# Optimization experiments

Hardware: AMD Instinct MI355X
Metric: run time of the kernel (lower is better)

## Reference

```python
import jax, jax.numpy as jnp
import numpy as np

TIME_PENALTY = 0.01
PONDER_EPS = 0.01
TIME_LIMIT = 16
BATCH, INPUT_SIZE, HIDDEN_SIZE = 4096, 1024, 1024


def setup_inputs() -> dict:
    key = jax.random.key(0)
    ks = jax.random.split(key, 8)
    s_in = 1.0 / np.sqrt(INPUT_SIZE + 1)
    s_h = 1.0 / np.sqrt(HIDDEN_SIZE)
    return {
        "inputs": jax.random.normal(ks[0], (BATCH, INPUT_SIZE), jnp.float32),
        "hidden": jax.random.normal(ks[1], (BATCH, HIDDEN_SIZE), jnp.float32),
        # RNNCell params (input size = INPUT_SIZE + 1 for the first-step flag)
        "W_ih": jax.random.uniform(ks[2], (HIDDEN_SIZE, INPUT_SIZE + 1), jnp.float32, -s_in, s_in),
        "b_ih": jax.random.uniform(ks[3], (HIDDEN_SIZE,), jnp.float32, -s_in, s_in),
        "W_hh": jax.random.uniform(ks[4], (HIDDEN_SIZE, HIDDEN_SIZE), jnp.float32, -s_h, s_h),
        "b_hh": jax.random.uniform(ks[5], (HIDDEN_SIZE,), jnp.float32, -s_h, s_h),
        # halting unit: Linear(hidden_size, 1), bias initialized to -1.0
        "W_halt": jax.random.uniform(ks[6], (1, HIDDEN_SIZE), jnp.float32, -s_h, s_h),
        "b_halt": jnp.full((1,), -1.0, jnp.float32),
    }


def _act_forward(inputs, hidden, W_ih, b_ih, W_hh, b_hh, W_halt, b_halt):
    B = inputs.shape[0]
    H = W_hh.shape[0]
    dt = inputs.dtype
    budget = jnp.asarray(1.0 - PONDER_EPS, dt)
    # input projection: the last input column is the first-step flag, so
    # step_inputs @ W_ih^T == inputs @ W_ih[:, :-1]^T + flag * W_ih[:, -1]
    x_base = inputs @ W_ih[:, :-1].T + b_ih  # (B, H)
    flag_col = W_ih[:, -1]                    # (H,)
    flags = (jnp.arange(TIME_LIMIT - 1) == 0).astype(dt)

    def step(carry, flag):
        h, halt_accum, cont, tot_h, tot_rem, tot_steps = carry
        h = jnp.tanh(x_base + flag * flag_col + h @ W_hh.T + b_hh)  # (B, H)
        step_halt = jax.nn.sigmoid(h @ W_halt.T + b_halt)           # (B, 1)
        masked_halt = jnp.where(cont, step_halt, 0.0)
        # halt accumulator is detached in the original (torch.no_grad)
        halt_accum = halt_accum + jax.lax.stop_gradient(masked_halt)
        ending = cont & (halt_accum + step_halt > budget)
        cont = cont & (~ending)
        tot_steps = tot_steps + cont.astype(dt)
        masked_rem = jnp.where(ending, 1.0 - halt_accum, 0.0)
        combined = masked_halt + masked_rem
        tot_h = tot_h + combined * h
        tot_rem = tot_rem + masked_halt
        return (h, halt_accum, cont, tot_h, tot_rem, tot_steps), None

    init = (
        hidden,
        jnp.zeros((B, 1), dt),
        jnp.ones((B, 1), bool),
        jnp.zeros((B, H), dt),
        jnp.zeros((B, 1), dt),
        jnp.zeros((B, 1), dt),
    )
    (h, halt_accum, cont, tot_h, tot_rem, tot_steps), _ = jax.lax.scan(step, init, flags)
    # for-else branch: elements still continuing after the loop get the remainder
    # (zero-contribution if everything halted early, matching the early break)
    tot_h = tot_h + jnp.where(cont, 1.0 - halt_accum, 0.0) * h
    ponder_cost = -TIME_PENALTY * tot_rem.mean()
    return tot_h, ponder_cost, tot_steps + 1.0


def reference(inputs, hidden, W_ih, b_ih, W_hh, b_hh, W_halt, b_halt):
    return _act_forward(inputs, hidden, W_ih, b_ih, W_hh, b_hh, W_halt, b_halt)
```

## Files before the change

kernel.cpp:

```cpp
#include <hip/hip_runtime.h>
#include <math.h>

#define BATCH 4096
#define HID   1024
#define KDIM  1024
#define NSTEP 15
#define KV    3072
#define NCHUNK (KV / 64)

#define TMM 128
#define TNN 64
#define LDAH 72

typedef _Float16 half8 __attribute__((ext_vector_type(8)));
typedef float floatx4 __attribute__((ext_vector_type(4)));

__device__ __forceinline__ _Float16 f16hi(float x) { return (_Float16)x; }

__global__ __launch_bounds__(256) void setup_kernel(
    const float* __restrict__ W_ih, const float* __restrict__ W_hh,
    const float* __restrict__ inputs, const float* __restrict__ hidden,
    _Float16* __restrict__ B3ih, _Float16* __restrict__ B3hh,
    _Float16* __restrict__ Ihi, _Float16* __restrict__ Ilo,
    _Float16* __restrict__ Hhi, _Float16* __restrict__ Hlo,
    float* __restrict__ flagcol, int* __restrict__ list0, int* __restrict__ counts,
    float* __restrict__ halt_accum, float* __restrict__ tot_rem) {
    size_t idx = (size_t)blockIdx.x * 256 + threadIdx.x;
    {
        float x = inputs[idx];
        _Float16 h = f16hi(x);
        Ihi[idx] = h; Ilo[idx] = (_Float16)(x - (float)h);
        float y = hidden[idx];
        _Float16 g = f16hi(y);
        Hhi[idx] = g; Hlo[idx] = (_Float16)(y - (float)g);
    }
    if (idx < (size_t)KDIM * KDIM) {
        int n = (int)(idx >> 10), k = (int)(idx & 1023);
        float w = W_hh[idx];
        _Float16 hi = f16hi(w);
        _Float16 lo = (_Float16)(w - (float)hi);
        size_t base = (size_t)n * KV;
        B3hh[base + k] = hi; B3hh[base + 1024 + k] = lo; B3hh[base + 2048 + k] = hi;
        float w2 = W_ih[(size_t)n * 1025 + k];
        _Float16 hi2 = f16hi(w2);
        _Float16 lo2 = (_Float16)(w2 - (float)hi2);
        B3ih[base + k] = hi2; B3ih[base + 1024 + k] = lo2; B3ih[base + 2048 + k] = hi2;
    }
    if (idx < BATCH) { list0[idx] = idx; halt_accum[idx] = 0.f; tot_rem[idx] = 0.f; }
    if (idx < KDIM) flagcol[idx] = W_ih[idx * 1025 + 1024];
    if (idx < 16) counts[idx] = (idx == 0) ? BATCH : 0;
}

__global__ __launch_bounds__(256) void mfma_step_kernel(
    const _Float16* __restrict__ Ahi, const _Float16* __restrict__ Alo,
    const _Float16* __restrict__ B3, const float* __restrict__ bias,
    const float* __restrict__ xbase, const float* __restrict__ flagcol, float flag,
    const int* __restrict__ list, const int* __restrict__ pcount,
    float* __restrict__ hout, _Float16* __restrict__ houthi, _Float16* __restrict__ houtlo,
    float* __restrict__ xout, int mode) {
    int count = pcount ? *pcount : BATCH;
    int row0 = blockIdx.x * TMM;
    if (row0 >= count) return;
    int col0 = blockIdx.y * TNN;

    __shared__ _Float16 Asm[2][TMM][LDAH];
    __shared__ _Float16 Bsm[2][TNN][LDAH];

    int t = threadIdx.x;
    int lane = t & 63, w = t >> 6;
    int wm = (w & 1) * 64, wn = (w >> 1) * 32;

    int arw[4], aq8[4]; size_t aoff[4];
#pragma unroll
    for (int l = 0; l < 4; l++) {
        int q = t + l * 256;
        int r = q >> 3, qk = q & 7;
        arw[l] = r; aq8[l] = qk * 8;
        int rr = row0 + r;
        int g = (rr < count) ? (list ? list[rr] : rr) : 0;
        aoff[l] = (size_t)g * KDIM + qk * 8;
    }
    int brw[2], bq8[2]; size_t boff[2];
#pragma unroll
    for (int l = 0; l < 2; l++) {
        int q = t + l * 256;
        int r = q >> 3, qk = q & 7;
        brw[l] = r; bq8[l] = qk * 8;
        boff[l] = (size_t)(col0 + r) * KV + qk * 8;
    }

    floatx4 acc[4][2];
#pragma unroll
    for (int i = 0; i < 4; i++)
#pragma unroll
        for (int j = 0; j < 2; j++) acc[i][j] = (floatx4)(0.f);

    int l15 = lane & 15, l4 = lane >> 4;

    half8 av[4], bv[2];
#pragma unroll
    for (int l = 0; l < 4; l++) av[l] = *(const half8*)(Ahi + aoff[l]);
#pragma unroll
    for (int l = 0; l < 2; l++) bv[l] = *(const half8*)(B3 + boff[l]);
#pragma unroll
    for (int l = 0; l < 4; l++) *(half8*)(&Asm[0][arw[l]][aq8[l]]) = av[l];
#pragma unroll
    for (int l = 0; l < 2; l++) *(half8*)(&Bsm[0][brw[l]][bq8[l]]) = bv[l];
    __syncthreads();

    int p = 0;
    for (int it = 0; it < NCHUNK; it++) {
        if (it + 1 < NCHUNK) {
            int k0v = (it + 1) << 6;
            const _Float16* Asrc = (k0v < 2048) ? Ahi : Alo;
            int kp = k0v & 1023;
#pragma unroll
            for (int l = 0; l < 4; l++) av[l] = *(const half8*)(Asrc + aoff[l] + kp);
#pragma unroll
            for (int l = 0; l < 2; l++) bv[l] = *(const half8*)(B3 + boff[l] + k0v);
        }
#pragma unroll
        for (int ks = 0; ks < 2; ks++) {
            int ko = ks * 32 + l4 * 8;
            half8 af[4], bf[2];
#pragma unroll
            for (int fi = 0; fi < 4; fi++)
                af[fi] = *(const half8*)(&Asm[p][wm + fi * 16 + l15][ko]);
#pragma unroll
            for (int fj = 0; fj < 2; fj++)
                bf[fj] = *(const half8*)(&Bsm[p][wn + fj * 16 + l15][ko]);
#pragma unroll
            for (int fi = 0; fi < 4; fi++)
#pragma unroll
                for (int fj = 0; fj < 2; fj++)
                    acc[fi][fj] = __builtin_amdgcn_mfma_f32_16x16x32_f16(
                        af[fi], bf[fj], acc[fi][fj], 0, 0, 0);
        }
        if (it + 1 < NCHUNK) {
            int q = p ^ 1;
#pragma unroll
            for (int l = 0; l < 4; l++) *(half8*)(&Asm[q][arw[l]][aq8[l]]) = av[l];
#pragma unroll
            for (int l = 0; l < 2; l++) *(half8*)(&Bsm[q][brw[l]][bq8[l]]) = bv[l];
        }
        __syncthreads();
        p ^= 1;
    }

#pragma unroll
    for (int fi = 0; fi < 4; fi++) {
#pragma unroll
        for (int rr = 0; rr < 4; rr++) {
            int lm = wm + fi * 16 + l4 * 4 + rr;
            int grd = row0 + lm;
            if (grd >= count) continue;
            int g = list ? list[grd] : grd;
#pragma unroll
            for (int fj = 0; fj < 2; fj++) {
                int c = col0 + wn + fj * 16 + l15;
                float v = acc[fi][fj][rr];
                if (mode == 0) {
                    xout[(size_t)g * KDIM + c] = v + bias[c];
                } else {
                    v += xbase[(size_t)g * KDIM + c] + flag * flagcol[c] + bias[c];
                    v = tanhf(v);
                    hout[(size_t)g * KDIM + c] = v;
                    _Float16 hi = f16hi(v);
                    houthi[(size_t)g * KDIM + c] = hi;
                    houtlo[(size_t)g * KDIM + c] = (_Float16)(v - (float)hi);
                }
            }
        }
    }
}

__global__ __launch_bounds__(256) void halt_kernel(
    const float* __restrict__ h, const float* __restrict__ W_halt,
    const float* __restrict__ b_halt,
    const int* __restrict__ list, const int* __restrict__ pcount,
    int* __restrict__ list_next, int* __restrict__ pcount_next,
    float* __restrict__ halt_accum, float* __restrict__ tot_rem,
    float* __restrict__ tot_h, float* __restrict__ steps_out,
    int stepnum, int first) {
    int count = *pcount;
    int wid = threadIdx.x >> 6, lane = threadIdx.x & 63;
    int r = blockIdx.x * 4 + wid;
    if (r >= count) return;
    int row = list[r];
    const float* hr = h + (size_t)row * HID;

    float dot = 0.f;
#pragma unroll
    for (int q = 0; q < 4; q++) {
        int c = q * 256 + lane * 4;
        float4 hv = *(const float4*)(hr + c);
        float4 wv = *(const float4*)(W_halt + c);
        dot += hv.x * wv.x + hv.y * wv.y + hv.z * wv.z + hv.w * wv.w;
    }
#pragma unroll
    for (int off = 32; off > 0; off >>= 1) dot += __shfl_down(dot, off);

    float combined = 0.f;
    if (lane == 0) {
        float p = 1.f / (1.f + expf(-(dot + b_halt[0])));
        float S = halt_accum[row] + p;
        halt_accum[row] = S;
        tot_rem[row] += p;
        bool ending = (S + p) > 0.99f;
        if (ending) {
            combined = p + (1.f - S);
            steps_out[row] = (float)stepnum;
        } else {
            combined = p;
            int idx = atomicAdd(pcount_next, 1);
            list_next[idx] = row;
        }
    }
    combined = __shfl(combined, 0);

    float* th = tot_h + (size_t)row * HID;
#pragma unroll
    for (int q = 0; q < 4; q++) {
        int c = q * 256 + lane * 4;
        float4 hv = *(const float4*)(hr + c);
        float4 ov;
        if (first) {
            ov.x = combined * hv.x; ov.y = combined * hv.y;
            ov.z = combined * hv.z; ov.w = combined * hv.w;
        } else {
            ov = *(const float4*)(th + c);
            ov.x += combined * hv.x; ov.y += combined * hv.y;
            ov.z += combined * hv.z; ov.w += combined * hv.w;
        }
        *(float4*)(th + c) = ov;
    }
}

__global__ __launch_bounds__(256) void epilogue_kernel(
    const float* __restrict__ h, const int* __restrict__ list,
    const int* __restrict__ pcount, const float* __restrict__ halt_accum,
    const float* __restrict__ tot_rem,
    float* __restrict__ tot_h, float* __restrict__ steps_out,
    float* __restrict__ ponder) {
    if (blockIdx.x == 1024) {
        __shared__ float red[4];
        int t = threadIdx.x;
        float v = 0.f;
#pragma unroll
        for (int i = 0; i < 16; i++) v += tot_rem[t + i * 256];
#pragma unroll
        for (int off = 32; off > 0; off >>= 1) v += __shfl_down(v, off);
        int lane = t & 63, wid = t >> 6;
        if (lane == 0) red[wid] = v;
        __syncthreads();
        if (t == 0) ponder[0] = (red[0] + red[1] + red[2] + red[3]) * (-0.01f / 4096.f);
        return;
    }
    int count = *pcount;
    int wid = threadIdx.x >> 6, lane = threadIdx.x & 63;
    int r = blockIdx.x * 4 + wid;
    if (r >= count) return;
    int row = list[r];
    float cmb = 1.f - halt_accum[row];
    if (lane == 0) steps_out[row] = 16.f;
    const float* hr = h + (size_t)row * HID;
    float* th = tot_h + (size_t)row * HID;
#pragma unroll
    for (int q = 0; q < 4; q++) {
        int c = q * 256 + lane * 4;
        float4 hv = *(const float4*)(hr + c);
        float4 ov = *(const float4*)(th + c);
        ov.x += cmb * hv.x; ov.y += cmb * hv.y;
        ov.z += cmb * hv.z; ov.w += cmb * hv.w;
        *(float4*)(th + c) = ov;
    }
}

extern "C" void kernel_launch(void* const* d_in, const int* in_sizes, int n_in,
                              void* d_out, int out_size, void* d_ws, size_t ws_size,
                              hipStream_t stream) {
    const float* inputs = (const float*)d_in[0];
    const float* hidden = (const float*)d_in[1];
    const float* W_ih   = (const float*)d_in[2];
    const float* b_ih   = (const float*)d_in[3];
    const float* W_hh   = (const float*)d_in[4];
    const float* b_hh   = (const float*)d_in[5];
    const float* W_halt = (const float*)d_in[6];
    const float* b_halt = (const float*)d_in[7];
    float* out = (float*)d_out;

    float* ws = (float*)d_ws;
    const size_t NM = (size_t)BATCH * HID;
    float* xbase = ws;
    float* h     = xbase + NM;
    _Float16* B3ih = (_Float16*)(h + NM);
    _Float16* B3hh = B3ih + (size_t)HID * KV;
    _Float16* Ahi0 = B3hh + (size_t)HID * KV;
    _Float16* Alo0 = Ahi0 + NM;
    _Float16* Ahi1 = Alo0 + NM;
    _Float16* Alo1 = Ahi1 + NM;
    float* flagcol = (float*)(Alo1 + NM);
    float* halt_accum = flagcol + KDIM;
    float* tot_rem = halt_accum + BATCH;
    int* list0 = (int*)(tot_rem + BATCH);
    int* list1 = list0 + BATCH;
    int* counts = list1 + BATCH;

    _Float16* Ahi[2] = {Ahi0, Ahi1};
    _Float16* Alo[2] = {Alo0, Alo1};
    int* lists[2] = {list0, list1};

    float* tot_h = out;
    float* ponder = out + NM;
    float* steps_out = ponder + 1;

    setup_kernel<<<16384, 256, 0, stream>>>(W_ih, W_hh, inputs, hidden,
                                            B3ih, B3hh, Ahi1, Alo1, Ahi0, Alo0,
                                            flagcol, list0, counts, halt_accum, tot_rem);

    mfma_step_kernel<<<dim3(32, 16), 256, 0, stream>>>(
        Ahi1, Alo1, B3ih, b_ih, nullptr, nullptr, 0.f, nullptr, nullptr,
        nullptr, nullptr, nullptr, xbase, 0);

    for (int t = 0; t < NSTEP; t++) {
        mfma_step_kernel<<<dim3(32, 16), 256, 0, stream>>>(
            Ahi[t & 1], Alo[t & 1], B3hh, b_hh, xbase, flagcol,
            (t == 0) ? 1.f : 0.f, lists[t & 1], counts + t,
            h, Ahi[(t + 1) & 1], Alo[(t + 1) & 1], nullptr, 1);
        halt_kernel<<<1024, 256, 0, stream>>>(h, W_halt, b_halt,
                                              lists[t & 1], counts + t,
                                              lists[(t + 1) & 1], counts + t + 1,
                                              halt_accum, tot_rem, tot_h, steps_out,
                                              t + 1, (t == 0) ? 1 : 0);
    }
    epilogue_kernel<<<1025, 256, 0, stream>>>(h, lists[1], counts + 15,
                                              halt_accum, tot_rem, tot_h, steps_out, ponder);
}
```

Before: 736.3 us.

## Deepen GEMM prefetch to two register stages with LDS-only barriers

Reworks the GEMM main loop to keep two chunks of global loads in flight, using even and odd register sets, so global latency is hidden across two MFMA chunks instead of one. It also replaces __syncthreads with a custom barrier that waits only on LDS counters (lgkmcnt) and not on outstanding global loads. This lets prefetched global loads stay pending across barriers. The cost is more register pressure from the extra staging buffers, which could lower occupancy.

```diff
diff --git a/kernel.cpp b/kernel.cpp
--- a/kernel.cpp
+++ b/kernel.cpp
@@ -16,6 +16,12 @@
 typedef float floatx4 __attribute__((ext_vector_type(4)));
 
 __device__ __forceinline__ _Float16 f16hi(float x) { return (_Float16)x; }
+
+__device__ __forceinline__ void barrier_ls() {
+    asm volatile("s_waitcnt lgkmcnt(0)" ::: "memory");
+    __builtin_amdgcn_s_barrier();
+    asm volatile("" ::: "memory");
+}
 
 __global__ __launch_bounds__(256) void setup_kernel(
     const float* __restrict__ W_ih, const float* __restrict__ W_hh,
@@ -97,55 +103,65 @@
 
     int l15 = lane & 15, l4 = lane >> 4;
 
-    half8 av[4], bv[2];
-#pragma unroll
-    for (int l = 0; l < 4; l++) av[l] = *(const half8*)(Ahi + aoff[l]);
-#pragma unroll
-    for (int l = 0; l < 2; l++) bv[l] = *(const half8*)(B3 + boff[l]);
-#pragma unroll
-    for (int l = 0; l < 4; l++) *(half8*)(&Asm[0][arw[l]][aq8[l]]) = av[l];
-#pragma unroll
-    for (int l = 0; l < 2; l++) *(half8*)(&Bsm[0][brw[l]][bq8[l]]) = bv[l];
-    __syncthreads();
-
-    int p = 0;
-    for (int it = 0; it < NCHUNK; it++) {
-        if (it + 1 < NCHUNK) {
-            int k0v = (it + 1) << 6;
-            const _Float16* Asrc = (k0v < 2048) ? Ahi : Alo;
-            int kp = k0v & 1023;
-#pragma unroll
-            for (int l = 0; l < 4; l++) av[l] = *(const half8*)(Asrc + aoff[l] + kp);
-#pragma unroll
-            for (int l = 0; l < 2; l++) bv[l] = *(const half8*)(B3 + boff[l] + k0v);
-        }
-#pragma unroll
-        for (int ks = 0; ks < 2; ks++) {
-            int ko = ks * 32 + l4 * 8;
-            half8 af[4], bf[2];
-#pragma unroll
-            for (int fi = 0; fi < 4; fi++)
-                af[fi] = *(const half8*)(&Asm[p][wm + fi * 16 + l15][ko]);
-#pragma unroll
-            for (int fj = 0; fj < 2; fj++)
-                bf[fj] = *(const half8*)(&Bsm[p][wn + fj * 16 + l15][ko]);
-#pragma unroll
-            for (int fi = 0; fi < 4; fi++)
-#pragma unroll
-                for (int fj = 0; fj < 2; fj++)
-                    acc[fi][fj] = __builtin_amdgcn_mfma_f32_16x16x32_f16(
-                        af[fi], bf[fj], acc[fi][fj], 0, 0, 0);
-        }
-        if (it + 1 < NCHUNK) {
-            int q = p ^ 1;
-#pragma unroll
-            for (int l = 0; l < 4; l++) *(half8*)(&Asm[q][arw[l]][aq8[l]]) = av[l];
-#pragma unroll
-            for (int l = 0; l < 2; l++) *(half8*)(&Bsm[q][brw[l]][bq8[l]]) = bv[l];
-        }
-        __syncthreads();
-        p ^= 1;
-    }
+    half8 avE[4], bvE[2];
+    half8 avO[4], bvO[2];
+
+#define ISSUE(avS, bvS, c) do {                                               \
+        int k0v_ = (c) << 6;                                                  \
+        const _Float16* Asrc_ = (k0v_ < 2048) ? Ahi : Alo;  \
+        int kp_ = k0v_ & 1023;                                                \
+        _Pragma("unroll")                                                     \
+        for (int l = 0; l < 4; l++) avS[l] = *(const half8*)(Asrc_ + aoff[l] + kp_); \
+        _Pragma("unroll")                                                     \
+        for (int l = 0; l < 2; l++) bvS[l] = *(const half8*)(B3 + boff[l] + k0v_);   \
+    } while (0)
+
+#define LDSW(buf, avS, bvS) do {                                              \
+        _Pragma("unroll")                                                     \
+        for (int l = 0; l < 4; l++) *(half8*)(&Asm[buf][arw[l]][aq8[l]]) = avS[l]; \
+        _Pragma("unroll")                                                     \
+        for (int l = 0; l < 2; l++) *(half8*)(&Bsm[buf][brw[l]][bq8[l]]) = bvS[l]; \
+    } while (0)
+
+#define MFMA_CHUNK(buf) do {                                                  \
+        _Pragma("unroll")                                                     \
+        for (int ks = 0; ks < 2; ks++) {                                      \
+            int ko = ks * 32 + l4 * 8;                                        \
+            half8 af[4], bf[2];                                               \
+            _Pragma("unroll")                                                 \
+            for (int fi = 0; fi < 4; fi++)                                    \
+                af[fi] = *(const half8*)(&Asm[buf][wm + fi * 16 + l15][ko]);  \
+            _Pragma("unroll")                                                 \
+            for (int fj = 0; fj < 2; fj++)                                    \
+                bf[fj] = *(const half8*)(&Bsm[buf][wn + fj * 16 + l15][ko]);  \
+            _Pragma("unroll")                                                 \
+            for (int fi = 0; fi < 4; fi++)                                    \
+                _Pragma("unroll")                                             \
+                for (int fj = 0; fj < 2; fj++)                                \
+                    acc[fi][fj] = __builtin_amdgcn_mfma_f32_16x16x32_f16(     \
+                        af[fi], bf[fj], acc[fi][fj], 0, 0, 0);                \
+        }                                                                     \
+    } while (0)
+
+    ISSUE(avE, bvE, 0);
+    ISSUE(avO, bvO, 1);
+    LDSW(0, avE, bvE);
+    barrier_ls();
+
+    for (int it = 0; it < NCHUNK; it += 2) {
+        if (it + 2 < NCHUNK) ISSUE(avE, bvE, it + 2);
+        MFMA_CHUNK(0);
+        LDSW(1, avO, bvO);
+        barrier_ls();
+        if (it + 3 < NCHUNK) ISSUE(avO, bvO, it + 3);
+        MFMA_CHUNK(1);
+        if (it + 2 < NCHUNK) LDSW(0, avE, bvE);
+        barrier_ls();
+    }
+
+#undef ISSUE
+#undef LDSW
+#undef MFMA_CHUNK
 
 #pragma unroll
     for (int fi = 0; fi < 4; fi++) {
```

New measurement: 738.5 us. About the same (+0.3%).

## Add per-wave tiled GEMM path for small active-row counts in step kernel

Applied to the files above, without the earlier changes.

The recurrent step kernel now switches on the active-row count. Above a threshold it keeps the shared-memory 128x64 block tile. Below it, each wavefront independently computes a 64x64 tile, reading operands straight from global memory with a three-stage register prefetch and no LDS or barriers. This spreads the shrinking tail batches across more independent waves to improve utilisation once many rows have halted. The cost is more register pressure in the fused kernel and redundant global loads that are not shared through LDS.

```diff
diff --git a/kernel.cpp b/kernel.cpp
--- a/kernel.cpp
+++ b/kernel.cpp
@@ -7,6 +7,7 @@
 #define NSTEP 15
 #define KV    3072
 #define NCHUNK (KV / 64)
+#define TAILTHRESH 1536
 
 #define TMM 128
 #define TNN 64
@@ -59,115 +60,207 @@
     float* __restrict__ hout, _Float16* __restrict__ houthi, _Float16* __restrict__ houtlo,
     float* __restrict__ xout, int mode) {
     int count = pcount ? *pcount : BATCH;
-    int row0 = blockIdx.x * TMM;
-    if (row0 >= count) return;
-    int col0 = blockIdx.y * TNN;
+    int t = threadIdx.x;
+    int lane = t & 63, w = t >> 6;
+    int l15 = lane & 15, l4 = lane >> 4;
 
     __shared__ _Float16 Asm[2][TMM][LDAH];
     __shared__ _Float16 Bsm[2][TNN][LDAH];
 
-    int t = threadIdx.x;
-    int lane = t & 63, w = t >> 6;
-    int wm = (w & 1) * 64, wn = (w >> 1) * 32;
-
-    int arw[4], aq8[4]; size_t aoff[4];
-#pragma unroll
-    for (int l = 0; l < 4; l++) {
-        int q = t + l * 256;
-        int r = q >> 3, qk = q & 7;
-        arw[l] = r; aq8[l] = qk * 8;
-        int rr = row0 + r;
-        int g = (rr < count) ? (list ? list[rr] : rr) : 0;
-        aoff[l] = (size_t)g * KDIM + qk * 8;
-    }
-    int brw[2], bq8[2]; size_t boff[2];
-#pragma unroll
-    for (int l = 0; l < 2; l++) {
-        int q = t + l * 256;
-        int r = q >> 3, qk = q & 7;
-        brw[l] = r; bq8[l] = qk * 8;
-        boff[l] = (size_t)(col0 + r) * KV + qk * 8;
-    }
-
-    floatx4 acc[4][2];
-#pragma unroll
-    for (int i = 0; i < 4; i++)
-#pragma unroll
-        for (int j = 0; j < 2; j++) acc[i][j] = (floatx4)(0.f);
-
-    int l15 = lane & 15, l4 = lane >> 4;
-
-    half8 av[4], bv[2];
-#pragma unroll
-    for (int l = 0; l < 4; l++) av[l] = *(const half8*)(Ahi + aoff[l]);
-#pragma unroll
-    for (int l = 0; l < 2; l++) bv[l] = *(const half8*)(B3 + boff[l]);
-#pragma unroll
-    for (int l = 0; l < 4; l++) *(half8*)(&Asm[0][arw[l]][aq8[l]]) = av[l];
-#pragma unroll
-    for (int l = 0; l < 2; l++) *(half8*)(&Bsm[0][brw[l]][bq8[l]]) = bv[l];
-    __syncthreads();
-
-    int p = 0;
-    for (int it = 0; it < NCHUNK; it++) {
-        if (it + 1 < NCHUNK) {
-            int k0v = (it + 1) << 6;
-            const _Float16* Asrc = (k0v < 2048) ? Ahi : Alo;
-            int kp = k0v & 1023;
-#pragma unroll
-            for (int l = 0; l < 4; l++) av[l] = *(const half8*)(Asrc + aoff[l] + kp);
-#pragma unroll
-            for (int l = 0; l < 2; l++) bv[l] = *(const half8*)(B3 + boff[l] + k0v);
-        }
-#pragma unroll
-        for (int ks = 0; ks < 2; ks++) {
-            int ko = ks * 32 + l4 * 8;
-            half8 af[4], bf[2];
-#pragma unroll
-            for (int fi = 0; fi < 4; fi++)
-                af[fi] = *(const half8*)(&Asm[p][wm + fi * 16 + l15][ko]);
-#pragma unroll
-            for (int fj = 0; fj < 2; fj++)
-                bf[fj] = *(const half8*)(&Bsm[p][wn + fj * 16 + l15][ko]);
-#pragma unroll
-            for (int fi = 0; fi < 4; fi++)
+    if (count >= TAILTHRESH) {
+        int bx = blockIdx.x & 31, by = blockIdx.x >> 5;
+        int row0 = bx * TMM;
+        if (row0 >= count) return;
+        int col0 = by * TNN;
+        int wm = (w & 1) * 64, wn = (w >> 1) * 32;
+
+        int arw[4], aq8[4]; size_t aoff[4];
+#pragma unroll
+        for (int l = 0; l < 4; l++) {
+            int q = t + l * 256;
+            int r = q >> 3, qk = q & 7;
+            arw[l] = r; aq8[l] = qk * 8;
+            int rr = row0 + r;
+            int g = (rr < count) ? (list ? list[rr] : rr) : 0;
+            aoff[l] = (size_t)g * KDIM + qk * 8;
+        }
+        int brw[2], bq8[2]; size_t boff[2];
+#pragma unroll
+        for (int l = 0; l < 2; l++) {
+            int q = t + l * 256;
+            int r = q >> 3, qk = q & 7;
+            brw[l] = r; bq8[l] = qk * 8;
+            boff[l] = (size_t)(col0 + r) * KV + qk * 8;
+        }
+
+        floatx4 acc[4][2];
+#pragma unroll
+        for (int i = 0; i < 4; i++)
+#pragma unroll
+            for (int j = 0; j < 2; j++) acc[i][j] = (floatx4)(0.f);
+
+        half8 av[4], bv[2];
+#pragma unroll
+        for (int l = 0; l < 4; l++) av[l] = *(const half8*)(Ahi + aoff[l]);
+#pragma unroll
+        for (int l = 0; l < 2; l++) bv[l] = *(const half8*)(B3 + boff[l]);
+#pragma unroll
+        for (int l = 0; l < 4; l++) *(half8*)(&Asm[0][arw[l]][aq8[l]]) = av[l];
+#pragma unroll
+        for (int l = 0; l < 2; l++) *(half8*)(&Bsm[0][brw[l]][bq8[l]]) = bv[l];
+        __syncthreads();
+
+        int p = 0;
+        for (int it = 0; it < NCHUNK; it++) {
+            if (it + 1 < NCHUNK) {
+                int k0v = (it + 1) << 6;
+                const _Float16* Asrc = (k0v < 2048) ? Ahi : Alo;
+                int kp = k0v & 1023;
+#pragma unroll
+                for (int l = 0; l < 4; l++) av[l] = *(const half8*)(Asrc + aoff[l] + kp);
+#pragma unroll
+                for (int l = 0; l < 2; l++) bv[l] = *(const half8*)(B3 + boff[l] + k0v);
+            }
+#pragma unroll
+            for (int ks = 0; ks < 2; ks++) {
+                int ko = ks * 32 + l4 * 8;
+                half8 af[4], bf[2];
+#pragma unroll
+                for (int fi = 0; fi < 4; fi++)
+                    af[fi] = *(const half8*)(&Asm[p][wm + fi * 16 + l15][ko]);
 #pragma unroll
                 for (int fj = 0; fj < 2; fj++)
-                    acc[fi][fj] = __builtin_amdgcn_mfma_f32_16x16x32_f16(
-                        af[fi], bf[fj], acc[fi][fj], 0, 0, 0);
-        }
-        if (it + 1 < NCHUNK) {
-            int q = p ^ 1;
-#pragma unroll
-            for (int l = 0; l < 4; l++) *(half8*)(&Asm[q][arw[l]][aq8[l]]) = av[l];
-#pragma unroll
-            for (int l = 0; l < 2; l++) *(half8*)(&Bsm[q][brw[l]][bq8[l]]) = bv[l];
-        }
-        __syncthreads();
-        p ^= 1;
-    }
-
-#pragma unroll
-    for (int fi = 0; fi < 4; fi++) {
-#pragma unroll
-        for (int rr = 0; rr < 4; rr++) {
-            int lm = wm + fi * 16 + l4 * 4 + rr;
-            int grd = row0 + lm;
-            if (grd >= count) continue;
-            int g = list ? list[grd] : grd;
-#pragma unroll
-            for (int fj = 0; fj < 2; fj++) {
-                int c = col0 + wn + fj * 16 + l15;
-                float v = acc[fi][fj][rr];
-                if (mode == 0) {
-                    xout[(size_t)g * KDIM + c] = v + bias[c];
-                } else {
-                    v += xbase[(size_t)g * KDIM + c] + flag * flagcol[c] + bias[c];
-                    v = tanhf(v);
-                    hout[(size_t)g * KDIM + c] = v;
-                    _Float16 hi = f16hi(v);
-                    houthi[(size_t)g * KDIM + c] = hi;
-                    houtlo[(size_t)g * KDIM + c] = (_Float16)(v - (float)hi);
+                    bf[fj] = *(const half8*)(&Bsm[p][wn + fj * 16 + l15][ko]);
+#pragma unroll
+                for (int fi = 0; fi < 4; fi++)
+#pragma unroll
+                    for (int fj = 0; fj < 2; fj++)
+                        acc[fi][fj] = __builtin_amdgcn_mfma_f32_16x16x32_f16(
+                            af[fi], bf[fj], acc[fi][fj], 0, 0, 0);
+            }
+            if (it + 1 < NCHUNK) {
+                int q = p ^ 1;
+#pragma unroll
+                for (int l = 0; l < 4; l++) *(half8*)(&Asm[q][arw[l]][aq8[l]]) = av[l];
+#pragma unroll
+                for (int l = 0; l < 2; l++) *(half8*)(&Bsm[q][brw[l]][bq8[l]]) = bv[l];
+            }
+            __syncthreads();
+            p ^= 1;
+        }
+
+#pragma unroll
+        for (int fi = 0; fi < 4; fi++) {
+#pragma unroll
+            for (int rr = 0; rr < 4; rr++) {
+                int lm = wm + fi * 16 + l4 * 4 + rr;
+                int grd = row0 + lm;
+                if (grd >= count) continue;
+                int g = list ? list[grd] : grd;
+#pragma unroll
+                for (int fj = 0; fj < 2; fj++) {
+                    int c = col0 + wn + fj * 16 + l15;
+                    float v = acc[fi][fj][rr];
+                    if (mode == 0) {
+                        xout[(size_t)g * KDIM + c] = v + bias[c];
+                    } else {
+                        v += xbase[(size_t)g * KDIM + c] + flag * flagcol[c] + bias[c];
+                        v = tanhf(v);
+                        hout[(size_t)g * KDIM + c] = v;
+                        _Float16 hi = f16hi(v);
+                        houthi[(size_t)g * KDIM + c] = hi;
+                        houtlo[(size_t)g * KDIM + c] = (_Float16)(v - (float)hi);
+                    }
+                }
+            }
+        }
+    } else {
+        int tid = w * 512 + blockIdx.x;
+        int bx = tid >> 4, by = tid & 15;
+        int row0 = bx * 64;
+        if (row0 >= count) return;
+        int col0 = by * 64;
+        int koff = l4 * 8;
+
+        size_t abase[4], bbase[4];
+#pragma unroll
+        for (int f = 0; f < 4; f++) {
+            int grow = row0 + f * 16 + l15;
+            int g = (grow < count) ? (list ? list[grow] : grow) : 0;
+            abase[f] = (size_t)g * KDIM + koff;
+            bbase[f] = (size_t)(col0 + f * 16 + l15) * KV + koff;
+        }
+
+        floatx4 acc[4][4];
+#pragma unroll
+        for (int i = 0; i < 4; i++)
+#pragma unroll
+            for (int j = 0; j < 4; j++) acc[i][j] = (floatx4)(0.f);
+
+        half8 avA[4][2], bvA[4][2], avB[4][2], bvB[4][2], avC[4][2], bvC[4][2];
+
+#define TISSUE(av, bv, c) do {                                                \
+        int k0v_ = (c) << 6;                                                  \
+        const _Float16* As_ = (k0v_ < 2048) ? Ahi : Alo;                      \
+        int kp_ = k0v_ & 1023;                                                \
+        _Pragma("unroll")                                                     \
+        for (int f = 0; f < 4; f++) {                                         \
+            _Pragma("unroll")                                                 \
+            for (int ks = 0; ks < 2; ks++) {                                  \
+                av[f][ks] = *(const half8*)(As_ + abase[f] + kp_ + ks * 32);  \
+                bv[f][ks] = *(const half8*)(B3 + bbase[f] + k0v_ + ks * 32);  \
+            }                                                                 \
+        }                                                                     \
+    } while (0)
+
+#define TMFMA(av, bv) do {                                                    \
+        _Pragma("unroll")                                                     \
+        for (int ks = 0; ks < 2; ks++)                                        \
+            _Pragma("unroll")                                                 \
+            for (int fi = 0; fi < 4; fi++)                                    \
+                _Pragma("unroll")                                             \
+                for (int fj = 0; fj < 4; fj++)                                \
+                    acc[fi][fj] = __builtin_amdgcn_mfma_f32_16x16x32_f16(     \
+                        av[fi][ks], bv[fj][ks], acc[fi][fj], 0, 0, 0);        \
+    } while (0)
+
+        TISSUE(avA, bvA, 0);
+        TISSUE(avB, bvB, 1);
+        TISSUE(avC, bvC, 2);
+
+        for (int it = 0; it < NCHUNK; it += 3) {
+            TMFMA(avA, bvA);
+            if (it + 3 < NCHUNK) TISSUE(avA, bvA, it + 3);
+            TMFMA(avB, bvB);
+            if (it + 4 < NCHUNK) TISSUE(avB, bvB, it + 4);
+            TMFMA(avC, bvC);
+            if (it + 5 < NCHUNK) TISSUE(avC, bvC, it + 5);
+        }
+#undef TISSUE
+#undef TMFMA
+
+#pragma unroll
+        for (int fi = 0; fi < 4; fi++) {
+#pragma unroll
+            for (int rr = 0; rr < 4; rr++) {
+                int lm = fi * 16 + l4 * 4 + rr;
+                int grd = row0 + lm;
+                if (grd >= count) continue;
+                int g = list ? list[grd] : grd;
+#pragma unroll
+                for (int fj = 0; fj < 4; fj++) {
+                    int c = col0 + fj * 16 + l15;
+                    float v = acc[fi][fj][rr];
+                    if (mode == 0) {
+                        xout[(size_t)g * KDIM + c] = v + bias[c];
+                    } else {
+                        v += xbase[(size_t)g * KDIM + c] + flag * flagcol[c] + bias[c];
+                        v = tanhf(v);
+                        hout[(size_t)g * KDIM + c] = v;
+                        _Float16 hi = f16hi(v);
+                        houthi[(size_t)g * KDIM + c] = hi;
+                        houtlo[(size_t)g * KDIM + c] = (_Float16)(v - (float)hi);
+                    }
                 }
             }
         }
@@ -318,12 +411,12 @@
                                             B3ih, B3hh, Ahi1, Alo1, Ahi0, Alo0,
                                             flagcol, list0, counts, halt_accum, tot_rem);
 
-    mfma_step_kernel<<<dim3(32, 16), 256, 0, stream>>>(
+    mfma_step_kernel<<<512, 256, 0, stream>>>(
         Ahi1, Alo1, B3ih, b_ih, nullptr, nullptr, 0.f, nullptr, nullptr,
         nullptr, nullptr, nullptr, xbase, 0);
 
     for (int t = 0; t < NSTEP; t++) {
-        mfma_step_kernel<<<dim3(32, 16), 256, 0, stream>>>(
+        mfma_step_kernel<<<512, 256, 0, stream>>>(
             Ahi[t & 1], Alo[t & 1], B3hh, b_hh, xbase, flagcol,
             (t == 0) ? 1.f : 0.f, lists[t & 1], counts + t,
             h, Ahi[(t + 1) & 1], Alo[(t + 1) & 1], nullptr, 1);
```

Result: slower. 909.9 us (+23.6%).

## Split-K the recurrent GEMM when few rows remain active, fuse reduction into halt kernel

Applied to the files above, without the earlier changes.

When fewer than 2048 rows are still active, the recurrent GEMM is split four ways along K over a third grid dimension. Each split writes partial sums to a workspace, and the halt kernel then reduces them, applies the bias and tanh, writes the fp16 hi/lo copies and computes the halting dot product in one pass. The aim is to fill the GPU when the active batch shrinks to a few tiles. The cost is extra partial-sum traffic, a larger grid whose blocks exit early in the full-batch steps, and an epilogue that rebuilds h from the fp16 hi/lo pair. In tail steps the fp32 h is no longer written, so the epilogue reads only the hi/lo halves.

```diff
diff --git a/kernel.cpp b/kernel.cpp
--- a/kernel.cpp
+++ b/kernel.cpp
@@ -1,5 +1,6 @@
 #include <hip/hip_runtime.h>
 #include <math.h>
+#include <stdint.h>
 
 #define BATCH 4096
 #define HID   1024
@@ -7,12 +8,16 @@
 #define NSTEP 15
 #define KV    3072
 #define NCHUNK (KV / 64)
+#define TAILTHRESH 2048
+#define SKT 4
+#define CPB (NCHUNK / SKT)
 
 #define TMM 128
 #define TNN 64
 #define LDAH 72
 
 typedef _Float16 half8 __attribute__((ext_vector_type(8)));
+typedef _Float16 half4v __attribute__((ext_vector_type(4)));
 typedef float floatx4 __attribute__((ext_vector_type(4)));
 
 __device__ __forceinline__ _Float16 f16hi(float x) { return (_Float16)x; }
@@ -57,11 +62,16 @@
     const float* __restrict__ xbase, const float* __restrict__ flagcol, float flag,
     const int* __restrict__ list, const int* __restrict__ pcount,
     float* __restrict__ hout, _Float16* __restrict__ houthi, _Float16* __restrict__ houtlo,
-    float* __restrict__ xout, int mode) {
+    float* __restrict__ xout, float* __restrict__ psplit, int mode) {
     int count = pcount ? *pcount : BATCH;
+    bool tail = (count < TAILTHRESH);
+    int bz = blockIdx.z;
+    if (!tail && bz != 0) return;
     int row0 = blockIdx.x * TMM;
     if (row0 >= count) return;
     int col0 = blockIdx.y * TNN;
+    int c0 = tail ? bz * CPB : 0;
+    int c1 = tail ? c0 + CPB : NCHUNK;
 
     __shared__ _Float16 Asm[2][TMM][LDAH];
     __shared__ _Float16 Bsm[2][TNN][LDAH];
@@ -98,10 +108,15 @@
     int l15 = lane & 15, l4 = lane >> 4;
 
     half8 av[4], bv[2];
-#pragma unroll
-    for (int l = 0; l < 4; l++) av[l] = *(const half8*)(Ahi + aoff[l]);
-#pragma unroll
-    for (int l = 0; l < 2; l++) bv[l] = *(const half8*)(B3 + boff[l]);
+    {
+        int k0v0 = c0 << 6;
+        const _Float16* As0 = (k0v0 < 2048) ? Ahi : Alo;
+        int kp0 = k0v0 & 1023;
+#pragma unroll
+        for (int l = 0; l < 4; l++) av[l] = *(const half8*)(As0 + aoff[l] + kp0);
+#pragma unroll
+        for (int l = 0; l < 2; l++) bv[l] = *(const half8*)(B3 + boff[l] + k0v0);
+    }
 #pragma unroll
     for (int l = 0; l < 4; l++) *(half8*)(&Asm[0][arw[l]][aq8[l]]) = av[l];
 #pragma unroll
@@ -109,8 +124,8 @@
     __syncthreads();
 
     int p = 0;
-    for (int it = 0; it < NCHUNK; it++) {
-        if (it + 1 < NCHUNK) {
+    for (int it = c0; it < c1; it++) {
+        if (it + 1 < c1) {
             int k0v = (it + 1) << 6;
             const _Float16* Asrc = (k0v < 2048) ? Ahi : Alo;
             int kp = k0v & 1023;
@@ -136,7 +151,7 @@
                     acc[fi][fj] = __builtin_amdgcn_mfma_f32_16x16x32_f16(
                         af[fi], bf[fj], acc[fi][fj], 0, 0, 0);
         }
-        if (it + 1 < NCHUNK) {
+        if (it + 1 < c1) {
             int q = p ^ 1;
 #pragma unroll
             for (int l = 0; l < 4; l++) *(half8*)(&Asm[q][arw[l]][aq8[l]]) = av[l];
@@ -147,6 +162,7 @@
         p ^= 1;
     }
 
+    float* pout = psplit + (size_t)bz * ((size_t)TAILTHRESH * KDIM);
 #pragma unroll
     for (int fi = 0; fi < 4; fi++) {
 #pragma unroll
@@ -154,20 +170,24 @@
             int lm = wm + fi * 16 + l4 * 4 + rr;
             int grd = row0 + lm;
             if (grd >= count) continue;
-            int g = list ? list[grd] : grd;
 #pragma unroll
             for (int fj = 0; fj < 2; fj++) {
                 int c = col0 + wn + fj * 16 + l15;
                 float v = acc[fi][fj][rr];
-                if (mode == 0) {
-                    xout[(size_t)g * KDIM + c] = v + bias[c];
+                if (tail) {
+                    pout[(size_t)grd * KDIM + c] = v;
                 } else {
-                    v += xbase[(size_t)g * KDIM + c] + flag * flagcol[c] + bias[c];
-                    v = tanhf(v);
-                    hout[(size_t)g * KDIM + c] = v;
-                    _Float16 hi = f16hi(v);
-                    houthi[(size_t)g * KDIM + c] = hi;
-                    houtlo[(size_t)g * KDIM + c] = (_Float16)(v - (float)hi);
+                    int g = list ? list[grd] : grd;
+                    if (mode == 0) {
+                        xout[(size_t)g * KDIM + c] = v + bias[c];
+                    } else {
+                        v += xbase[(size_t)g * KDIM + c] + flag * flagcol[c] + bias[c];
+                        v = tanhf(v);
+                        hout[(size_t)g * KDIM + c] = v;
+                        _Float16 hi = f16hi(v);
+                        houthi[(size_t)g * KDIM + c] = hi;
+                        houtlo[(size_t)g * KDIM + c] = (_Float16)(v - (float)hi);
+                    }
                 }
             }
         }
@@ -181,21 +201,93 @@
     int* __restrict__ list_next, int* __restrict__ pcount_next,
     float* __restrict__ halt_accum, float* __restrict__ tot_rem,
     float* __restrict__ tot_h, float* __restrict__ steps_out,
-    int stepnum, int first) {
+    int stepnum, int first,
+    const float* __restrict__ xbase, const float* __restrict__ b_hh,
+    const float* __restrict__ psplit,
+    _Float16* __restrict__ houthi, _Float16* __restrict__ houtlo) {
     int count = *pcount;
     int wid = threadIdx.x >> 6, lane = threadIdx.x & 63;
     int r = blockIdx.x * 4 + wid;
     if (r >= count) return;
     int row = list[r];
+
+    if (count < TAILTHRESH) {
+        const size_t PSTR = (size_t)TAILTHRESH * KDIM;
+        const float* p0 = psplit;
+        const float* p1 = psplit + PSTR;
+        const float* p2 = psplit + 2 * PSTR;
+        const float* p3 = psplit + 3 * PSTR;
+        const float* xr = xbase + (size_t)row * HID;
+        size_t rb = (size_t)r * KDIM;
+        size_t gb = (size_t)row * HID;
+        float4 hv[4];
+        float dot = 0.f;
+#pragma unroll
+        for (int q = 0; q < 4; q++) {
+            int c = q * 256 + lane * 4;
+            float4 x = *(const float4*)(xr + c);
+            float4 bb = *(const float4*)(b_hh + c);
+            float4 s0 = *(const float4*)(p0 + rb + c);
+            float4 s1 = *(const float4*)(p1 + rb + c);
+            float4 s2 = *(const float4*)(p2 + rb + c);
+            float4 s3 = *(const float4*)(p3 + rb + c);
+            float4 hh;
+            hh.x = tanhf(x.x + bb.x + s0.x + s1.x + s2.x + s3.x);
+            hh.y = tanhf(x.y + bb.y + s0.y + s1.y + s2.y + s3.y);
+            hh.z = tanhf(x.z + bb.z + s0.z + s1.z + s2.z + s3.z);
+            hh.w = tanhf(x.w + bb.w + s0.w + s1.w + s2.w + s3.w);
+            hv[q] = hh;
+            float4 wv = *(const float4*)(W_halt + c);
+            dot += hh.x * wv.x + hh.y * wv.y + hh.z * wv.z + hh.w * wv.w;
+            half4v hi4, lo4;
+            hi4[0] = f16hi(hh.x); lo4[0] = (_Float16)(hh.x - (float)hi4[0]);
+            hi4[1] = f16hi(hh.y); lo4[1] = (_Float16)(hh.y - (float)hi4[1]);
+            hi4[2] = f16hi(hh.z); lo4[2] = (_Float16)(hh.z - (float)hi4[2]);
+            hi4[3] = f16hi(hh.w); lo4[3] = (_Float16)(hh.w - (float)hi4[3]);
+            *(half4v*)(houthi + gb + c) = hi4;
+            *(half4v*)(houtlo + gb + c) = lo4;
+        }
+#pragma unroll
+        for (int off = 32; off > 0; off >>= 1) dot += __shfl_down(dot, off);
+
+        float combined = 0.f;
+        if (lane == 0) {
+            float p = 1.f / (1.f + expf(-(dot + b_halt[0])));
+            float S = halt_accum[row] + p;
+            halt_accum[row] = S;
+            tot_rem[row] += p;
+            bool ending = (S + p) > 0.99f;
+            if (ending) {
+                combined = p + (1.f - S);
+                steps_out[row] = (float)stepnum;
+            } else {
+                combined = p;
+                int idx = atomicAdd(pcount_next, 1);
+                list_next[idx] = row;
+            }
+        }
+        combined = __shfl(combined, 0);
+
+        float* th = tot_h + gb;
+#pragma unroll
+        for (int q = 0; q < 4; q++) {
+            int c = q * 256 + lane * 4;
+            float4 ov = *(const float4*)(th + c);
+            ov.x += combined * hv[q].x; ov.y += combined * hv[q].y;
+            ov.z += combined * hv[q].z; ov.w += combined * hv[q].w;
+            *(float4*)(th + c) = ov;
+        }
+        return;
+    }
+
     const float* hr = h + (size_t)row * HID;
-
     float dot = 0.f;
 #pragma unroll
     for (int q = 0; q < 4; q++) {
         int c = q * 256 + lane * 4;
-        float4 hv = *(const float4*)(hr + c);
+        float4 hvv = *(const float4*)(hr + c);
         float4 wv = *(const float4*)(W_halt + c);
-        dot += hv.x * wv.x + hv.y * wv.y + hv.z * wv.z + hv.w * wv.w;
+        dot += hvv.x * wv.x + hvv.y * wv.y + hvv.z * wv.z + hvv.w * wv.w;
     }
 #pragma unroll
     for (int off = 32; off > 0; off >>= 1) dot += __shfl_down(dot, off);
@@ -222,22 +314,23 @@
 #pragma unroll
     for (int q = 0; q < 4; q++) {
         int c = q * 256 + lane * 4;
-        float4 hv = *(const float4*)(hr + c);
+        float4 hvv = *(const float4*)(hr + c);
         float4 ov;
         if (first) {
-            ov.x = combined * hv.x; ov.y = combined * hv.y;
-            ov.z = combined * hv.z; ov.w = combined * hv.w;
+            ov.x = combined * hvv.x; ov.y = combined * hvv.y;
+            ov.z = combined * hvv.z; ov.w = combined * hvv.w;
         } else {
             ov = *(const float4*)(th + c);
-            ov.x += combined * hv.x; ov.y += combined * hv.y;
-            ov.z += combined * hv.z; ov.w += combined * hv.w;
+            ov.x += combined * hvv.x; ov.y += combined * hvv.y;
+            ov.z += combined * hvv.z; ov.w += combined * hvv.w;
         }
         *(float4*)(th + c) = ov;
     }
 }
 
 __global__ __launch_bounds__(256) void epilogue_kernel(
-    const float* __restrict__ h, const int* __restrict__ list,
+    const _Float16* __restrict__ hhi, const _Float16* __restrict__ hlo,
+    const int* __restrict__ list,
     const int* __restrict__ pcount, const float* __restrict__ halt_accum,
     const float* __restrict__ tot_rem,
     float* __restrict__ tot_h, float* __restrict__ steps_out,
@@ -263,15 +356,19 @@
     int row = list[r];
     float cmb = 1.f - halt_accum[row];
     if (lane == 0) steps_out[row] = 16.f;
-    const float* hr = h + (size_t)row * HID;
+    const _Float16* hih = hhi + (size_t)row * HID;
+    const _Float16* loh = hlo + (size_t)row * HID;
     float* th = tot_h + (size_t)row * HID;
 #pragma unroll
     for (int q = 0; q < 4; q++) {
         int c = q * 256 + lane * 4;
-        float4 hv = *(const float4*)(hr + c);
+        half4v hi4 = *(const half4v*)(hih + c);
+        half4v lo4 = *(const half4v*)(loh + c);
         float4 ov = *(const float4*)(th + c);
-        ov.x += cmb * hv.x; ov.y += cmb * hv.y;
-        ov.z += cmb * hv.z; ov.w += cmb * hv.w;
+        ov.x += cmb * ((float)hi4[0] + (float)lo4[0]);
+        ov.y += cmb * ((float)hi4[1] + (float)lo4[1]);
+        ov.z += cmb * ((float)hi4[2] + (float)lo4[2]);
+        ov.w += cmb * ((float)hi4[3] + (float)lo4[3]);
         *(float4*)(th + c) = ov;
     }
 }
@@ -305,6 +402,7 @@
     int* list0 = (int*)(tot_rem + BATCH);
     int* list1 = list0 + BATCH;
     int* counts = list1 + BATCH;
+    float* psplit = (float*)(counts + 16);
 
     _Float16* Ahi[2] = {Ahi0, Ahi1};
     _Float16* Alo[2] = {Alo0, Alo1};
@@ -318,21 +416,23 @@
                                             B3ih, B3hh, Ahi1, Alo1, Ahi0, Alo0,
                                             flagcol, list0, counts, halt_accum, tot_rem);
 
-    mfma_step_kernel<<<dim3(32, 16), 256, 0, stream>>>(
+    mfma_step_kernel<<<dim3(32, 16, SKT), 256, 0, stream>>>(
         Ahi1, Alo1, B3ih, b_ih, nullptr, nullptr, 0.f, nullptr, nullptr,
-        nullptr, nullptr, nullptr, xbase, 0);
+        nullptr, nullptr, nullptr, xbase, psplit, 0);
 
     for (int t = 0; t < NSTEP; t++) {
-        mfma_step_kernel<<<dim3(32, 16), 256, 0, stream>>>(
+        mfma_step_kernel<<<dim3(32, 16, SKT), 256, 0, stream>>>(
             Ahi[t & 1], Alo[t & 1], B3hh, b_hh, xbase, flagcol,
             (t == 0) ? 1.f : 0.f, lists[t & 1], counts + t,
-            h, Ahi[(t + 1) & 1], Alo[(t + 1) & 1], nullptr, 1);
+            h, Ahi[(t + 1) & 1], Alo[(t + 1) & 1], nullptr, psplit, 1);
         halt_kernel<<<1024, 256, 0, stream>>>(h, W_halt, b_halt,
                                               lists[t & 1], counts + t,
                                               lists[(t + 1) & 1], counts + t + 1,
                                               halt_accum, tot_rem, tot_h, steps_out,
-                                              t + 1, (t == 0) ? 1 : 0);
-    }
-    epilogue_kernel<<<1025, 256, 0, stream>>>(h, lists[1], counts + 15,
+                                              t + 1, (t == 0) ? 1 : 0,
+                                              xbase, b_hh, psplit,
+                                              Ahi[(t + 1) & 1], Alo[(t + 1) & 1]);
+    }
+    epilogue_kernel<<<1025, 256, 0, stream>>>(Ahi[1], Alo[1], lists[1], counts + 15,
                                               halt_accum, tot_rem, tot_h, steps_out, ponder);
 }
```

Measured after the change: 756.4 us. +2.7%, slower.
